# Kernel tuning notes

Measured on AMD Instinct MI355X. Metric: run time of the kernel, lower is better.

## Reference

```python
import jax, jax.numpy as jnp
import numpy as np

B, T, D_MODEL, N_HEADS = 2, 2048, 1024, 16
HEAD_DIM = D_MODEL // N_HEADS


def _ln(x, g, b, eps=1e-5):
    m = x.mean(-1, keepdims=True)
    v = ((x - m) ** 2).mean(-1, keepdims=True)
    return (x - m) / jnp.sqrt(v + eps) * g + b


def setup_inputs() -> dict:
    key = jax.random.key(0)
    ks = jax.random.split(key, 7)
    f = jnp.float32
    x = jax.random.normal(ks[0], (B, T, D_MODEL), f)
    Wq = jax.random.normal(ks[1], (D_MODEL, D_MODEL), f) * 0.02
    Wk = jax.random.normal(ks[2], (D_MODEL, D_MODEL), f) * 0.02
    Wv = jax.random.normal(ks[3], (D_MODEL, D_MODEL), f) * 0.02
    Wo = jax.random.normal(ks[4], (D_MODEL, D_MODEL), f) * 0.02
    return {
        'x': x, 'Wq': Wq, 'Wk': Wk, 'Wv': Wv, 'Wo': Wo,
        'evolution_rate': jnp.asarray(0.1, f),
        'memory_decay': jnp.asarray(0.85, f),
        'temporal_weights': jax.random.normal(ks[5], (HEAD_DIM,), f) * 0.02,
        'q_gamma': jnp.ones((HEAD_DIM,), f), 'q_beta': jnp.zeros((HEAD_DIM,), f),
        'k_gamma': jnp.ones((HEAD_DIM,), f), 'k_beta': jnp.zeros((HEAD_DIM,), f),
    }


def reference(x, Wq, Wk, Wv, Wo, evolution_rate, memory_decay,
              temporal_weights, q_gamma, q_beta, k_gamma, k_beta):
    b, t, c = x.shape
    h, d = N_HEADS, HEAD_DIM
    # projections (torch Linear: y = x @ W^T), split heads -> [B,H,T,D]
    q = jnp.einsum('btc,oc->bto', x, Wq).reshape(b, t, h, d).transpose(0, 2, 1, 3)
    k = jnp.einsum('btc,oc->bto', x, Wk).reshape(b, t, h, d).transpose(0, 2, 1, 3)
    v = jnp.einsum('btc,oc->bto', x, Wv).reshape(b, t, h, d).transpose(0, 2, 1, 3)

    sig_md = jax.nn.sigmoid(memory_decay)
    # temporal signal per position: sin(sigmoid(er)*(pos+1) * w)  -> [T,D]
    ef = jax.nn.sigmoid(evolution_rate) * jnp.arange(1, t + 1, dtype=x.dtype)
    ts = jnp.sin(ef[:, None] * temporal_weights[None, :])

    def step(mem, inp):  # mem: [B,H,D]
        q_t, k_t, ts_t = inp  # [B,H,D],[B,H,D],[D]
        eq = _ln(q_t + ts_t + sig_md * mem, q_gamma, q_beta)
        ek = _ln(k_t + 0.5 * ts_t + 0.3 * sig_md * mem, k_gamma, k_beta)
        return 0.7 * mem + 0.3 * q_t, (eq, ek)

    mem0 = jnp.zeros((b, h, d), x.dtype)
    qT = q.transpose(2, 0, 1, 3)  # [T,B,H,D]
    kT = k.transpose(2, 0, 1, 3)
    _, (eqT, ekT) = jax.lax.scan(step, mem0, (qT, kT, ts))
    eq = eqT.transpose(1, 2, 0, 3)  # [B,H,T,D]
    ek = ekT.transpose(1, 2, 0, 3)

    scale = 1.0 / np.sqrt(d).astype(np.float32)
    scores = jnp.einsum('bhtd,bhsd->bhts', eq, ek) * scale
    causal = jnp.tril(jnp.ones((t, t), bool))
    scores = jnp.where(causal[None, None], scores, -jnp.inf)
    w = jax.nn.softmax(scores, axis=-1)  # dropout is identity (eval)
    out = jnp.einsum('bhts,bhsd->bhtd', w, v)
    out = out.transpose(0, 2, 1, 3).reshape(b, t, c)
    return jnp.einsum('btc,oc->bto', out, Wo)
```

## Files before the change

kernel.cpp:

```cpp
#include <hip/hip_runtime.h>
#include <stdint.h>

#define T_SEQ   2048
#define NHEADS  16
#define HDIM    64
#define DMODEL  1024

typedef __attribute__((ext_vector_type(8))) _Float16 half8_t;
typedef __attribute__((ext_vector_type(4))) float    float4_t;

typedef __attribute__((address_space(1))) unsigned char ga_u8;
typedef __attribute__((address_space(3))) unsigned char lds_u8;

__device__ __forceinline__ unsigned short f2h(float f) {
  _Float16 h = (_Float16)f;
  return __builtin_bit_cast(unsigned short, h);
}
__device__ __forceinline__ float h2f(unsigned short u) {
  return (float)__builtin_bit_cast(_Float16, u);
}
__device__ __forceinline__ unsigned packh2(float a, float b) {
  return (unsigned)f2h(a) | ((unsigned)f2h(b) << 16);
}
__device__ __forceinline__ unsigned packu2(unsigned short a, unsigned short b) {
  return (unsigned)a | ((unsigned)b << 16);
}
__device__ __forceinline__ void async_copy16(const void* g, void* l) {
  __builtin_amdgcn_global_load_lds((ga_u8*)g, (lds_u8*)l, 16, 0, 0);
}

__global__ __launch_bounds__(256) void cvt_f32_f16(const float* __restrict__ s,
                                                   unsigned short* __restrict__ d, int n4) {
  int i = blockIdx.x * 256 + threadIdx.x;
  if (i >= n4) return;
  float4 v = ((const float4*)s)[i];
  ushort4 o;
  o.x = f2h(v.x); o.y = f2h(v.y); o.z = f2h(v.z); o.w = f2h(v.w);
  ((ushort4*)d)[i] = o;
}

__global__ __launch_bounds__(256) void cvt_weights(
    const float* __restrict__ w0, const float* __restrict__ w1,
    const float* __restrict__ w2, const float* __restrict__ w3,
    unsigned short* __restrict__ d0, unsigned short* __restrict__ d1,
    unsigned short* __restrict__ d2, unsigned short* __restrict__ d3, int n4) {
  int i = blockIdx.x * 256 + threadIdx.x;
  if (i >= n4) return;
  const float* s = (blockIdx.y == 0) ? w0 : (blockIdx.y == 1) ? w1 : (blockIdx.y == 2) ? w2 : w3;
  unsigned short* d = (blockIdx.y == 0) ? d0 : (blockIdx.y == 1) ? d1 : (blockIdx.y == 2) ? d2 : d3;
  float4 v = ((const float4*)s)[i];
  ushort4 o;
  o.x = f2h(v.x); o.y = f2h(v.y); o.z = f2h(v.z); o.w = f2h(v.w);
  ((ushort4*)d)[i] = o;
}

__global__ __launch_bounds__(256) void gemm_qkv(
    const unsigned short* __restrict__ A,
    const unsigned short* __restrict__ Bq, const unsigned short* __restrict__ Bk,
    const unsigned short* __restrict__ Bv,
    unsigned short* __restrict__ Cq, unsigned short* __restrict__ Ck,
    unsigned short* __restrict__ Cv) {
  const unsigned short* B = (blockIdx.z == 0) ? Bq : (blockIdx.z == 1) ? Bk : Bv;
  unsigned short*       C = (blockIdx.z == 0) ? Cq : (blockIdx.z == 1) ? Ck : Cv;

  __shared__ alignas(16) unsigned short As[128 * 32];
  __shared__ alignas(16) unsigned short Bs[128 * 32];
  const int tid  = threadIdx.x;
  const int lane = tid & 63, w = tid >> 6;
  const int c = lane & 15, g = lane >> 4;
  const int wr = w >> 1, wc = w & 1;
  const int m0 = blockIdx.y * 128, n0 = blockIdx.x * 128;

  float4_t acc[4][4];
#pragma unroll
  for (int m = 0; m < 4; ++m)
#pragma unroll
    for (int n = 0; n < 4; ++n) acc[m][n] = (float4_t){0.f, 0.f, 0.f, 0.f};

  for (int k0 = 0; k0 < 1024; k0 += 32) {
    __syncthreads();
#pragma unroll
    for (int r = 0; r < 2; ++r) {
      const int idx = r * 256 + tid;
      const int row = idx >> 2, kc = (idx & 3) * 8;
      async_copy16(A + (size_t)(m0 + row) * 1024 + k0 + kc, As + r * 2048 + w * 512);
      async_copy16(B + (size_t)(n0 + row) * 1024 + k0 + kc, Bs + r * 2048 + w * 512);
    }
    __syncthreads();
    half8_t af[4], bf[4];
#pragma unroll
    for (int m = 0; m < 4; ++m) af[m] = *(const half8_t*)&As[(wr * 64 + m * 16 + c) * 32 + g * 8];
#pragma unroll
    for (int n = 0; n < 4; ++n) bf[n] = *(const half8_t*)&Bs[(wc * 64 + n * 16 + c) * 32 + g * 8];
#pragma unroll
    for (int m = 0; m < 4; ++m)
#pragma unroll
      for (int n = 0; n < 4; ++n)
        acc[m][n] = __builtin_amdgcn_mfma_f32_16x16x32_f16(af[m], bf[n], acc[m][n], 0, 0, 0);
  }
#pragma unroll
  for (int m = 0; m < 4; ++m)
#pragma unroll
    for (int j = 0; j < 4; ++j) {
      const int row = m0 + wr * 64 + m * 16 + g * 4 + j;
#pragma unroll
      for (int n = 0; n < 4; ++n) {
        const int col = n0 + wc * 64 + n * 16 + c;
        C[(size_t)row * 1024 + col] = f2h(acc[m][n][j]);
      }
    }
}

__global__ __launch_bounds__(256) void gemm_nt_out(const unsigned short* __restrict__ A,
                                                   const unsigned short* __restrict__ B,
                                                   float* __restrict__ C) {
  __shared__ alignas(16) unsigned short As[128 * 32];
  __shared__ alignas(16) unsigned short Bs[128 * 32];
  const int tid  = threadIdx.x;
  const int lane = tid & 63, w = tid >> 6;
  const int c = lane & 15, g = lane >> 4;
  const int wr = w >> 1, wc = w & 1;
  const int m0 = blockIdx.y * 128, n0 = blockIdx.x * 128;

  float4_t acc[4][4];
#pragma unroll
  for (int m = 0; m < 4; ++m)
#pragma unroll
    for (int n = 0; n < 4; ++n) acc[m][n] = (float4_t){0.f, 0.f, 0.f, 0.f};

  for (int k0 = 0; k0 < 1024; k0 += 32) {
    __syncthreads();
#pragma unroll
    for (int r = 0; r < 2; ++r) {
      const int idx = r * 256 + tid;
      const int row = idx >> 2, kc = (idx & 3) * 8;
      async_copy16(A + (size_t)(m0 + row) * 1024 + k0 + kc, As + r * 2048 + w * 512);
      async_copy16(B + (size_t)(n0 + row) * 1024 + k0 + kc, Bs + r * 2048 + w * 512);
    }
    __syncthreads();
    half8_t af[4], bf[4];
#pragma unroll
    for (int m = 0; m < 4; ++m) af[m] = *(const half8_t*)&As[(wr * 64 + m * 16 + c) * 32 + g * 8];
#pragma unroll
    for (int n = 0; n < 4; ++n) bf[n] = *(const half8_t*)&Bs[(wc * 64 + n * 16 + c) * 32 + g * 8];
#pragma unroll
    for (int m = 0; m < 4; ++m)
#pragma unroll
      for (int n = 0; n < 4; ++n)
        acc[m][n] = __builtin_amdgcn_mfma_f32_16x16x32_f16(af[m], bf[n], acc[m][n], 0, 0, 0);
  }
#pragma unroll
  for (int m = 0; m < 4; ++m)
#pragma unroll
    for (int j = 0; j < 4; ++j) {
      const int row = m0 + wr * 64 + m * 16 + g * 4 + j;
#pragma unroll
      for (int n = 0; n < 4; ++n) {
        const int col = n0 + wc * 64 + n * 16 + c;
        C[(size_t)row * 1024 + col] = acc[m][n][j];
      }
    }
}

__global__ __launch_bounds__(64) void evolve_ln(
    const unsigned short* __restrict__ q, const unsigned short* __restrict__ k,
    const float* __restrict__ er_p, const float* __restrict__ md_p,
    const float* __restrict__ tw, const float* __restrict__ qgamma,
    const float* __restrict__ qbeta, const float* __restrict__ kgamma,
    const float* __restrict__ kbeta,
    unsigned short* __restrict__ eq, unsigned short* __restrict__ ek) {
  const int lane = threadIdx.x;
  const int t0 = blockIdx.x * 32;
  const int bh = blockIdx.y;
  const int b = bh >> 4, h = bh & 15;
  const float sig_er = 1.f / (1.f + expf(-er_p[0]));
  const float smd    = 1.f / (1.f + expf(-md_p[0]));
  const float wv = tw[lane];
  const float gq = qgamma[lane], bq = qbeta[lane];
  const float gk = kgamma[lane], bk = kbeta[lane];
  const size_t base = ((size_t)b * T_SEQ) * DMODEL + h * HDIM + lane;

  float mem = 0.f;
  const int start = (t0 >= 64) ? (t0 - 64) : 0;
  for (int t = start; t < t0; ++t)
    mem = 0.7f * mem + 0.3f * h2f(q[base + (size_t)t * DMODEL]);

  for (int t = t0; t < t0 + 32; ++t) {
    const float qv = h2f(q[base + (size_t)t * DMODEL]);
    const float kv = h2f(k[base + (size_t)t * DMODEL]);
    const float ts = sinf(sig_er * (float)(t + 1) * wv);
    const float xq = qv + ts + smd * mem;
    const float xk = kv + 0.5f * ts + 0.3f * smd * mem;
    float s1 = xq, s2 = xq * xq, s3 = xk, s4 = xk * xk;
#pragma unroll
    for (int off = 32; off > 0; off >>= 1) {
      s1 += __shfl_xor(s1, off);
      s2 += __shfl_xor(s2, off);
      s3 += __shfl_xor(s3, off);
      s4 += __shfl_xor(s4, off);
    }
    const float mq = s1 * (1.f / 64.f);
    const float vq = fmaxf(s2 * (1.f / 64.f) - mq * mq, 0.f);
    const float mk = s3 * (1.f / 64.f);
    const float vk = fmaxf(s4 * (1.f / 64.f) - mk * mk, 0.f);
    eq[base + (size_t)t * DMODEL] = f2h((xq - mq) * rsqrtf(vq + 1e-5f) * gq + bq);
    ek[base + (size_t)t * DMODEL] = f2h((xk - mk) * rsqrtf(vk + 1e-5f) * gk + bk);
    mem = 0.7f * mem + 0.3f * qv;
  }
}

__global__ __launch_bounds__(256) void attn_fused(
    const unsigned short* __restrict__ eq, const unsigned short* __restrict__ ek,
    const unsigned short* __restrict__ v, unsigned short* __restrict__ o) {
  __shared__ alignas(16) float Ssh[4][16][36];
  __shared__ float Alds[4][16];
  __shared__ float Llds[4][16];
  const int tid = threadIdx.x;
  const int lane = tid & 63, w = tid >> 6;
  const int c = lane & 15, g = lane >> 4;
  const int p = blockIdx.y * 4 + w;
  const int bh = blockIdx.x;
  const int b = bh >> 4, h = bh & 15;
  const size_t head = ((size_t)b * T_SEQ) * DMODEL + h * HDIM;

  for (int half = 0; half < 2; ++half) {
    const int sub = half ? (127 - p) : p;
    const int qw = sub * 16;
    const int qrow = qw + c;

    const half8_t aq0 = *(const half8_t*)(eq + head + (size_t)qrow * DMODEL + g * 8);
    const half8_t aq1 = *(const half8_t*)(eq + head + (size_t)qrow * DMODEL + 32 + g * 8);

    float4_t acc[4];
#pragma unroll
    for (int n = 0; n < 4; ++n) acc[n] = (float4_t){0.f, 0.f, 0.f, 0.f};
    float mrun = -1e30f, lsum = 0.f;

    const int ntiles = (qw >> 5) + 1;
    for (int tile = 0; tile < ntiles; ++tile) {
      const int s0 = tile * 32;
#pragma unroll
      for (int st = 0; st < 2; ++st) {
        const unsigned short* ekr = ek + head + (size_t)(s0 + st * 16 + c) * DMODEL;
        const half8_t bk0 = *(const half8_t*)(ekr + g * 8);
        const half8_t bk1 = *(const half8_t*)(ekr + 32 + g * 8);
        float4_t z = (float4_t){0.f, 0.f, 0.f, 0.f};
        z = __builtin_amdgcn_mfma_f32_16x16x32_f16(aq0, bk0, z, 0, 0, 0);
        z = __builtin_amdgcn_mfma_f32_16x16x32_f16(aq1, bk1, z, 0, 0, 0);
#pragma unroll
        for (int j = 0; j < 4; ++j)
          Ssh[w][g * 4 + j][st * 16 + c] = z[j] * 0.125f;
      }

      float pf[8];
      float tmax = -1e30f;
#pragma unroll
      for (int e = 0; e < 8; ++e) {
        const int sa = s0 + g * 8 + e;
        const float val = (sa <= qrow) ? Ssh[w][c][g * 8 + e] : -1e30f;
        pf[e] = val;
        tmax = fmaxf(tmax, val);
      }
      tmax = fmaxf(tmax, __shfl_xor(tmax, 16));
      tmax = fmaxf(tmax, __shfl_xor(tmax, 32));
      const float mnew = fmaxf(mrun, tmax);
      const float alpha = __expf(mrun - mnew);
      mrun = mnew;
      float psum = 0.f;
#pragma unroll
      for (int e = 0; e < 8; ++e) {
        pf[e] = __expf(pf[e] - mnew);
        psum += pf[e];
      }
      psum += __shfl_xor(psum, 16);
      psum += __shfl_xor(psum, 32);
      lsum = lsum * alpha + psum;
      if (g == 0) Alds[w][c] = alpha;

      uint4 pu;
      pu.x = packh2(pf[0], pf[1]);
      pu.y = packh2(pf[2], pf[3]);
      pu.z = packh2(pf[4], pf[5]);
      pu.w = packh2(pf[6], pf[7]);
      const half8_t pa = __builtin_bit_cast(half8_t, pu);

      float af[4];
#pragma unroll
      for (int j = 0; j < 4; ++j) af[j] = Alds[w][g * 4 + j];
#pragma unroll
      for (int n = 0; n < 4; ++n) {
        acc[n][0] *= af[0]; acc[n][1] *= af[1];
        acc[n][2] *= af[2]; acc[n][3] *= af[3];
      }
      const unsigned short* vp = v + head + (size_t)(s0 + g * 8) * DMODEL + c;
#pragma unroll
      for (int n = 0; n < 4; ++n) {
        const unsigned short* vq2 = vp + n * 16;
        uint4 bu;
        bu.x = packu2(vq2[0 * DMODEL], vq2[1 * DMODEL]);
        bu.y = packu2(vq2[2 * DMODEL], vq2[3 * DMODEL]);
        bu.z = packu2(vq2[4 * DMODEL], vq2[5 * DMODEL]);
        bu.w = packu2(vq2[6 * DMODEL], vq2[7 * DMODEL]);
        const half8_t bv = __builtin_bit_cast(half8_t, bu);
        acc[n] = __builtin_amdgcn_mfma_f32_16x16x32_f16(pa, bv, acc[n], 0, 0, 0);
      }
    }

    if (g == 0) Llds[w][c] = lsum;
    float lj[4];
#pragma unroll
    for (int j = 0; j < 4; ++j) lj[j] = 1.f / Llds[w][g * 4 + j];
#pragma unroll
    for (int n = 0; n < 4; ++n)
#pragma unroll
      for (int j = 0; j < 4; ++j)
        o[head + (size_t)(qw + g * 4 + j) * DMODEL + n * 16 + c] = f2h(acc[n][j] * lj[j]);
  }
}

extern "C" void kernel_launch(void* const* d_in, const int* in_sizes, int n_in,
                              void* d_out, int out_size, void* d_ws, size_t ws_size,
                              hipStream_t stream) {
  const float* x  = (const float*)d_in[0];
  const float* Wq = (const float*)d_in[1];
  const float* Wk = (const float*)d_in[2];
  const float* Wv = (const float*)d_in[3];
  const float* Wo = (const float*)d_in[4];
  const float* er = (const float*)d_in[5];
  const float* md = (const float*)d_in[6];
  const float* tw = (const float*)d_in[7];
  const float* qg = (const float*)d_in[8];
  const float* qb = (const float*)d_in[9];
  const float* kg = (const float*)d_in[10];
  const float* kb = (const float*)d_in[11];

  const size_t NX = (size_t)2 * T_SEQ * DMODEL;
  const size_t NW = (size_t)DMODEL * DMODEL;

  unsigned short* xh  = (unsigned short*)d_ws;
  unsigned short* woh = xh + NX;
  unsigned short* wqh = woh + NW;
  unsigned short* wkh = wqh + NW;
  unsigned short* wvh = wkh + NW;
  unsigned short* qh  = wvh + NW;
  unsigned short* kh  = qh + NX;
  unsigned short* vh  = kh + NX;
  unsigned short* ekh = vh + NX;
  unsigned short* aoh = ekh + NX;
  unsigned short* eqh = xh;

  const int n4x = (int)(NX / 4), n4w = (int)(NW / 4);

  cvt_f32_f16<<<n4x / 256, 256, 0, stream>>>(x, xh, n4x);
  cvt_weights<<<dim3(n4w / 256, 4), 256, 0, stream>>>(Wq, Wk, Wv, Wo,
                                                      wqh, wkh, wvh, woh, n4w);

  gemm_qkv<<<dim3(8, 32, 3), 256, 0, stream>>>(xh, wqh, wkh, wvh, qh, kh, vh);

  evolve_ln<<<dim3(T_SEQ / 32, 32), 64, 0, stream>>>(qh, kh, er, md, tw,
                                                     qg, qb, kg, kb, eqh, ekh);

  attn_fused<<<dim3(32, 16), 256, 0, stream>>>(eqh, ekh, vh, aoh);

  gemm_nt_out<<<dim3(8, 32), 256, 0, stream>>>(aoh, woh, (float*)d_out);
}
```

Baseline: 207.5 us.

## Pre-transpose V into key-block tiles so attention loads MFMA B operand vectorized

Adds a transpose kernel that rewrites V into per-head, per-32-key-block tiles laid out by head-dim row, stored in the now-unused Q buffer. The attention inner loop then fetches each MFMA B operand with a single 16-byte load instead of eight strided 2-byte gathers across rows. This costs one extra kernel launch plus a full read and write of V. The variable `tile` in attn_fused is assumed to be the key-block index.

```diff
diff --git a/kernel.cpp b/kernel.cpp
--- a/kernel.cpp
+++ b/kernel.cpp
@@ -209,9 +209,43 @@
   }
 }
 
+__global__ __launch_bounds__(256) void transpose_v(const unsigned short* __restrict__ v,
+                                                   unsigned short* __restrict__ vt) {
+  __shared__ alignas(16) unsigned short tile[64][72];
+  const int tid = threadIdx.x;
+  const int t0 = blockIdx.x * 64;
+  const int bh = blockIdx.y;
+  const int b = bh >> 4, h = bh & 15;
+  const size_t src = ((size_t)b * T_SEQ + t0) * DMODEL + h * HDIM;
+
+  const int r = tid >> 2, c0 = (tid & 3) * 16;
+  const int sw = ((r >> 4) & 3) << 4;
+  const uint4 a0 = *(const uint4*)(v + src + (size_t)r * DMODEL + c0);
+  const uint4 a1 = *(const uint4*)(v + src + (size_t)r * DMODEL + c0 + 8);
+  *(uint4*)&tile[r][c0 ^ sw] = a0;
+  *(uint4*)&tile[r][(c0 ^ sw) + 8] = a1;
+  __syncthreads();
+
+  const int dr = tid >> 2, tc = (tid & 3) * 16;
+  const int swr = ((tc >> 4) & 3) << 4;
+  unsigned short tmp[16];
+#pragma unroll
+  for (int j = 0; j < 16; ++j) tmp[j] = tile[tc + j][dr ^ swr];
+  uint4 o0, o1;
+  o0.x = packu2(tmp[0], tmp[1]);   o0.y = packu2(tmp[2], tmp[3]);
+  o0.z = packu2(tmp[4], tmp[5]);   o0.w = packu2(tmp[6], tmp[7]);
+  o1.x = packu2(tmp[8], tmp[9]);   o1.y = packu2(tmp[10], tmp[11]);
+  o1.z = packu2(tmp[12], tmp[13]); o1.w = packu2(tmp[14], tmp[15]);
+  const int blk = (t0 + tc) >> 5;
+  const int sl  = tc & 31;
+  const size_t dst = (((size_t)bh * 64 + blk) * 64 + dr) * 32 + sl;
+  *(uint4*)(vt + dst) = o0;
+  *(uint4*)(vt + dst + 8) = o1;
+}
+
 __global__ __launch_bounds__(256) void attn_fused(
     const unsigned short* __restrict__ eq, const unsigned short* __restrict__ ek,
-    const unsigned short* __restrict__ v, unsigned short* __restrict__ o) {
+    const unsigned short* __restrict__ vt, unsigned short* __restrict__ o) {
   __shared__ alignas(16) float Ssh[4][16][36];
   __shared__ float Alds[4][16];
   __shared__ float Llds[4][16];
@@ -292,16 +326,10 @@
         acc[n][0] *= af[0]; acc[n][1] *= af[1];
         acc[n][2] *= af[2]; acc[n][3] *= af[3];
       }
-      const unsigned short* vp = v + head + (size_t)(s0 + g * 8) * DMODEL + c;
+      const unsigned short* vtile = vt + (((size_t)bh * 64 + tile) * 64) * 32;
 #pragma unroll
       for (int n = 0; n < 4; ++n) {
-        const unsigned short* vq2 = vp + n * 16;
-        uint4 bu;
-        bu.x = packu2(vq2[0 * DMODEL], vq2[1 * DMODEL]);
-        bu.y = packu2(vq2[2 * DMODEL], vq2[3 * DMODEL]);
-        bu.z = packu2(vq2[4 * DMODEL], vq2[5 * DMODEL]);
-        bu.w = packu2(vq2[6 * DMODEL], vq2[7 * DMODEL]);
-        const half8_t bv = __builtin_bit_cast(half8_t, bu);
+        const half8_t bv = *(const half8_t*)(vtile + (n * 16 + c) * 32 + g * 8);
         acc[n] = __builtin_amdgcn_mfma_f32_16x16x32_f16(pa, bv, acc[n], 0, 0, 0);
       }
     }
@@ -348,6 +376,7 @@
   unsigned short* ekh = vh + NX;
   unsigned short* aoh = ekh + NX;
   unsigned short* eqh = xh;
+  unsigned short* vtb = qh;
 
   const int n4x = (int)(NX / 4), n4w = (int)(NW / 4);
 
@@ -360,7 +389,9 @@
   evolve_ln<<<dim3(T_SEQ / 32, 32), 64, 0, stream>>>(qh, kh, er, md, tw,
                                                      qg, qb, kg, kb, eqh, ekh);
 
-  attn_fused<<<dim3(32, 16), 256, 0, stream>>>(eqh, ekh, vh, aoh);
+  transpose_v<<<dim3(T_SEQ / 64, 32), 256, 0, stream>>>(vh, vtb);
+
+  attn_fused<<<dim3(32, 16), 256, 0, stream>>>(eqh, ekh, vtb, aoh);
 
   gemm_nt_out<<<dim3(8, 32), 256, 0, stream>>>(aoh, woh, (float*)d_out);
 }
```

Measured after the change: 211.8 us. 2.1% more time.

## Store V transposed in tiles for vector loads; shrink evolve_ln chunk

Applied to the files above, without the earlier changes.

The QKV GEMM now writes V in a per-head, per-32-token tiled transposed layout (d-major within each tile). The attention kernel can then fetch each MFMA B operand with one 16-byte load instead of eight strided 2-byte gathers. Separately, evolve_ln uses 16-token chunks with a 48-step warmup of the memory recurrence instead of 32 and 64, giving more blocks. The transposed V store scatters 2-byte writes, and the shorter warmup slightly changes how far the truncated recurrence approximation reaches (0.7^48 is still negligible).

```diff
diff --git a/kernel.cpp b/kernel.cpp
--- a/kernel.cpp
+++ b/kernel.cpp
@@ -21,9 +21,6 @@
 }
 __device__ __forceinline__ unsigned packh2(float a, float b) {
   return (unsigned)f2h(a) | ((unsigned)f2h(b) << 16);
-}
-__device__ __forceinline__ unsigned packu2(unsigned short a, unsigned short b) {
-  return (unsigned)a | ((unsigned)b << 16);
 }
 __device__ __forceinline__ void async_copy16(const void* g, void* l) {
   __builtin_amdgcn_global_load_lds((ga_u8*)g, (lds_u8*)l, 16, 0, 0);
@@ -59,9 +56,8 @@
     const unsigned short* __restrict__ Bq, const unsigned short* __restrict__ Bk,
     const unsigned short* __restrict__ Bv,
     unsigned short* __restrict__ Cq, unsigned short* __restrict__ Ck,
-    unsigned short* __restrict__ Cv) {
+    unsigned short* __restrict__ Cvt) {
   const unsigned short* B = (blockIdx.z == 0) ? Bq : (blockIdx.z == 1) ? Bk : Bv;
-  unsigned short*       C = (blockIdx.z == 0) ? Cq : (blockIdx.z == 1) ? Ck : Cv;
 
   __shared__ alignas(16) unsigned short As[128 * 32];
   __shared__ alignas(16) unsigned short Bs[128 * 32];
@@ -98,17 +94,36 @@
       for (int n = 0; n < 4; ++n)
         acc[m][n] = __builtin_amdgcn_mfma_f32_16x16x32_f16(af[m], bf[n], acc[m][n], 0, 0, 0);
   }
-#pragma unroll
-  for (int m = 0; m < 4; ++m)
-#pragma unroll
-    for (int j = 0; j < 4; ++j) {
-      const int row = m0 + wr * 64 + m * 16 + g * 4 + j;
-#pragma unroll
-      for (int n = 0; n < 4; ++n) {
-        const int col = n0 + wc * 64 + n * 16 + c;
-        C[(size_t)row * 1024 + col] = f2h(acc[m][n][j]);
-      }
-    }
+
+  if (blockIdx.z < 2) {
+    unsigned short* C = (blockIdx.z == 0) ? Cq : Ck;
+#pragma unroll
+    for (int m = 0; m < 4; ++m)
+#pragma unroll
+      for (int j = 0; j < 4; ++j) {
+        const int row = m0 + wr * 64 + m * 16 + g * 4 + j;
+#pragma unroll
+        for (int n = 0; n < 4; ++n) {
+          const int col = n0 + wc * 64 + n * 16 + c;
+          C[(size_t)row * 1024 + col] = f2h(acc[m][n][j]);
+        }
+      }
+  } else {
+#pragma unroll
+    for (int m = 0; m < 4; ++m)
+#pragma unroll
+      for (int j = 0; j < 4; ++j) {
+        const int row = m0 + wr * 64 + m * 16 + g * 4 + j;
+        const int b = row >> 11, t = row & 2047;
+#pragma unroll
+        for (int n = 0; n < 4; ++n) {
+          const int col = n0 + wc * 64 + n * 16 + c;
+          const int h = col >> 6, d = col & 63;
+          const size_t dst = ((((size_t)(b * NHEADS + h) * 64 + (t >> 5)) * 64 + d) << 5) + (t & 31);
+          Cvt[dst] = f2h(acc[m][n][j]);
+        }
+      }
+  }
 }
 
 __global__ __launch_bounds__(256) void gemm_nt_out(const unsigned short* __restrict__ A,
@@ -170,7 +185,7 @@
     const float* __restrict__ kbeta,
     unsigned short* __restrict__ eq, unsigned short* __restrict__ ek) {
   const int lane = threadIdx.x;
-  const int t0 = blockIdx.x * 32;
+  const int t0 = blockIdx.x * 16;
   const int bh = blockIdx.y;
   const int b = bh >> 4, h = bh & 15;
   const float sig_er = 1.f / (1.f + expf(-er_p[0]));
@@ -181,11 +196,11 @@
   const size_t base = ((size_t)b * T_SEQ) * DMODEL + h * HDIM + lane;
 
   float mem = 0.f;
-  const int start = (t0 >= 64) ? (t0 - 64) : 0;
+  const int start = (t0 >= 48) ? (t0 - 48) : 0;
   for (int t = start; t < t0; ++t)
     mem = 0.7f * mem + 0.3f * h2f(q[base + (size_t)t * DMODEL]);
 
-  for (int t = t0; t < t0 + 32; ++t) {
+  for (int t = t0; t < t0 + 16; ++t) {
     const float qv = h2f(q[base + (size_t)t * DMODEL]);
     const float kv = h2f(k[base + (size_t)t * DMODEL]);
     const float ts = sinf(sig_er * (float)(t + 1) * wv);
@@ -211,7 +226,7 @@
 
 __global__ __launch_bounds__(256) void attn_fused(
     const unsigned short* __restrict__ eq, const unsigned short* __restrict__ ek,
-    const unsigned short* __restrict__ v, unsigned short* __restrict__ o) {
+    const unsigned short* __restrict__ vt, unsigned short* __restrict__ o) {
   __shared__ alignas(16) float Ssh[4][16][36];
   __shared__ float Alds[4][16];
   __shared__ float Llds[4][16];
@@ -292,16 +307,10 @@
         acc[n][0] *= af[0]; acc[n][1] *= af[1];
         acc[n][2] *= af[2]; acc[n][3] *= af[3];
       }
-      const unsigned short* vp = v + head + (size_t)(s0 + g * 8) * DMODEL + c;
+      const unsigned short* vtile = vt + (((size_t)bh * 64 + tile) * 64) * 32;
 #pragma unroll
       for (int n = 0; n < 4; ++n) {
-        const unsigned short* vq2 = vp + n * 16;
-        uint4 bu;
-        bu.x = packu2(vq2[0 * DMODEL], vq2[1 * DMODEL]);
-        bu.y = packu2(vq2[2 * DMODEL], vq2[3 * DMODEL]);
-        bu.z = packu2(vq2[4 * DMODEL], vq2[5 * DMODEL]);
-        bu.w = packu2(vq2[6 * DMODEL], vq2[7 * DMODEL]);
-        const half8_t bv = __builtin_bit_cast(half8_t, bu);
+        const half8_t bv = *(const half8_t*)(vtile + (n * 16 + c) * 32 + g * 8);
         acc[n] = __builtin_amdgcn_mfma_f32_16x16x32_f16(pa, bv, acc[n], 0, 0, 0);
       }
     }
@@ -344,8 +353,8 @@
   unsigned short* wvh = wkh + NW;
   unsigned short* qh  = wvh + NW;
   unsigned short* kh  = qh + NX;
-  unsigned short* vh  = kh + NX;
-  unsigned short* ekh = vh + NX;
+  unsigned short* vtb = kh + NX;
+  unsigned short* ekh = vtb + NX;
   unsigned short* aoh = ekh + NX;
   unsigned short* eqh = xh;
 
@@ -355,12 +364,12 @@
   cvt_weights<<<dim3(n4w / 256, 4), 256, 0, stream>>>(Wq, Wk, Wv, Wo,
                                                       wqh, wkh, wvh, woh, n4w);
 
-  gemm_qkv<<<dim3(8, 32, 3), 256, 0, stream>>>(xh, wqh, wkh, wvh, qh, kh, vh);
-
-  evolve_ln<<<dim3(T_SEQ / 32, 32), 64, 0, stream>>>(qh, kh, er, md, tw,
+  gemm_qkv<<<dim3(8, 32, 3), 256, 0, stream>>>(xh, wqh, wkh, wvh, qh, kh, vtb);
+
+  evolve_ln<<<dim3(T_SEQ / 16, 32), 64, 0, stream>>>(qh, kh, er, md, tw,
                                                      qg, qb, kg, kb, eqh, ekh);
 
-  attn_fused<<<dim3(32, 16), 256, 0, stream>>>(eqh, ekh, vh, aoh);
+  attn_fused<<<dim3(32, 16), 256, 0, stream>>>(eqh, ekh, vtb, aoh);
 
   gemm_nt_out<<<dim3(8, 32), 256, 0, stream>>>(aoh, woh, (float*)d_out);
 }
```

After: 211.1 us. Within noise of the previous version (+1.8%).
